# Kernel optimization log

Measured on AMD Instinct MI355X. Metric: run time of the kernel, lower is better.

The kernel has to match this reference:

```python
import jax, jax.numpy as jnp
import numpy as np

B, C_IN, C_OUT, H, W = 8, 64, 64, 128, 128
KH = KW = 3
K = KH * KW
PAD = 1


def setup_inputs() -> dict:
    key = jax.random.key(0)
    k1, k2, k3, k4 = jax.random.split(key, 4)
    inputs = {
        "input": jax.random.normal(k1, (B, C_IN, H, W), dtype=jnp.float32),
        "offset_and_mask": jax.random.normal(k2, (B, 3 * K, H, W), dtype=jnp.float32),
        "weight": jax.random.normal(k3, (C_OUT, C_IN, KH, KW), dtype=jnp.float32) * (1.0 / np.sqrt(C_IN * K)),
        "bias": jax.random.normal(k4, (C_OUT,), dtype=jnp.float32) * 0.1,
    }
    return inputs


def _dcnv2(x, offset_and_mask, weight, bias):
    b, c, h, w = x.shape
    co = weight.shape[0]
    # offset layout: first 2K channels are (dy, dx) pairs per kernel point, last K are mask logits
    off = offset_and_mask[:, : 2 * K].reshape(b, K, 2, h, w)
    mask = jax.nn.sigmoid(offset_and_mask[:, 2 * K :])  # [b, K, h, w]

    # base sampling grid for 3x3 conv, stride 1, pad 1, dilation 1
    hh = jnp.arange(h, dtype=jnp.float32)
    ww = jnp.arange(w, dtype=jnp.float32)
    ky = (jnp.arange(K) // KW).astype(jnp.float32) - PAD  # [K]
    kx = (jnp.arange(K) % KW).astype(jnp.float32) - PAD
    base_y = hh[None, :, None] + ky[:, None, None]  # [K, h, 1]
    base_x = ww[None, None, :] + kx[:, None, None]  # [K, 1, w]
    ys = base_y + off[:, :, 0]  # [b, K, h, w]
    xs = base_x + off[:, :, 1]

    def sample_one(img, ys1, xs1):
        # img [c,h,w]; ys1, xs1 [K,h,w]; bilinear with zero padding outside
        y0 = jnp.floor(ys1).astype(jnp.int32)
        x0 = jnp.floor(xs1).astype(jnp.int32)
        y1, x1 = y0 + 1, x0 + 1
        wy = ys1 - y0.astype(jnp.float32)
        wx = xs1 - x0.astype(jnp.float32)
        img_flat = img.reshape(c, h * w)

        def gather(yi, xi):
            valid = ((yi >= 0) & (yi < h) & (xi >= 0) & (xi < w)).astype(img.dtype)
            flat = jnp.clip(yi, 0, h - 1) * w + jnp.clip(xi, 0, w - 1)  # [K,h,w]
            v = img_flat[:, flat.reshape(-1)].reshape(c, K, h, w)
            return v * valid[None]

        v00 = gather(y0, x0)
        v01 = gather(y0, x1)
        v10 = gather(y1, x0)
        v11 = gather(y1, x1)
        return (
            v00 * ((1 - wy) * (1 - wx))[None]
            + v01 * ((1 - wy) * wx)[None]
            + v10 * (wy * (1 - wx))[None]
            + v11 * (wy * wx)[None]
        )  # [c, K, h, w]

    sampled = jax.vmap(sample_one)(x, ys, xs)  # [b, c, K, h, w]
    sampled = sampled * mask[:, None]
    w_flat = weight.reshape(co, c, K)
    out = jnp.einsum("bckhw,ock->bohw", sampled, w_flat)
    return out + bias[None, :, None, None]


def reference(input, offset_and_mask, weight, bias):
    return _dcnv2(input, offset_and_mask, weight, bias)
```

## Files before the change

kernel.cpp:

```cpp
#include <hip/hip_runtime.h>

#define Bn 8
#define Cc 64
#define CO 64
#define Hh 128
#define Ww 128
#define Kk 9
#define HW (Hh*Ww)

typedef __attribute__((ext_vector_type(8))) short bf16x8;
typedef __attribute__((ext_vector_type(4))) float f32x4;

__device__ __forceinline__ short f2bf(float f) {
    unsigned u = __float_as_uint(f);
    u = (u + 0x7FFFu + ((u >> 16) & 1u)) >> 16;
    return (short)u;
}
__device__ __forceinline__ float bf2f(short s) {
    return __uint_as_float(((unsigned)(unsigned short)s) << 16);
}

__global__ __launch_bounds__(256) void transpose_in_kernel(
    const float* __restrict__ in, short* __restrict__ in_t)
{
    __shared__ float tile[64 * 65];
    int bid  = blockIdx.x;
    int xblk = bid & 1;
    int row  = bid >> 1;
    int y    = row & (Hh - 1);
    int b    = row >> 7;
    int x0   = xblk << 6;
    int t    = threadIdx.x;

    int x  = t & 63;
    int cq = t >> 6;
    const float* src = in + (size_t)b * Cc * HW + (size_t)y * Ww + x0;
#pragma unroll
    for (int i = 0; i < 16; ++i) {
        int c = cq * 16 + i;
        tile[c * 65 + x] = src[(size_t)c * HW + x];
    }
    __syncthreads();
    int c2 = t & 63;
    int xq = t >> 6;
    short* dst = in_t + ((size_t)(b * Hh + y) * Ww + x0) * Cc;
#pragma unroll
    for (int i = 0; i < 16; ++i) {
        int xx = xq * 16 + i;
        dst[(size_t)xx * Cc + c2] = f2bf(tile[c2 * 65 + xx]);
    }
}

__global__ __launch_bounds__(256) void prep_w_kernel(
    const float* __restrict__ w, short* __restrict__ w_t)
{
    int idx = blockIdx.x * 256 + threadIdx.x;
    if (idx < Kk * CO * Cc) {
        int k  = idx >> 12;
        int co = (idx >> 6) & 63;
        int c  = idx & 63;
        w_t[idx] = f2bf(w[((size_t)co * Cc + c) * Kk + k]);
    }
}

__global__ __launch_bounds__(256, 4) void dcn_main_kernel(
    const short* __restrict__ in_t,
    const float* __restrict__ offm,
    const short* __restrict__ w_t,
    const float* __restrict__ bias,
    float* __restrict__ out)
{
    __shared__ short s_S[2][64][72];
    __shared__ short s_W[2][64][72];

    int bid  = blockIdx.x;
    int xblk = bid & 1;
    int row  = bid >> 1;
    int y    = row & (Hh - 1);
    int b    = row >> 7;
    int x0   = xblk << 6;
    int t    = threadIdx.x;
    int l    = t & 63;
    int wv   = t >> 6;
    int p_sub = l >> 2;
    int chunk = l & 3;
    int px   = (wv << 4) + p_sub;

    const float* offb = offm + (size_t)b * 27 * HW + (size_t)y * Ww + x0 + px;
    const short* inb  = in_t + (size_t)b * HW * Cc;

    int wco = t >> 2;
    int wc0 = (t & 3) << 4;

    float offv[Kk][3];
#pragma unroll
    for (int k = 0; k < Kk; ++k) {
        offv[k][0] = offb[(size_t)(2 * k) * HW];
        offv[k][1] = offb[(size_t)(2 * k + 1) * HW];
        offv[k][2] = offb[(size_t)(18 + k) * HW];
    }

    f32x4 acc[4] = {{0.f,0.f,0.f,0.f},{0.f,0.f,0.f,0.f},{0.f,0.f,0.f,0.f},{0.f,0.f,0.f,0.f}};
    int lm = l & 15;
    int g  = l >> 4;

    bf16x8 r[4][2];
    float  cw[4];
    bf16x8 wr[2];

    auto stage_load = [&](int k) {
        float dy = offv[k][0], dx = offv[k][1], ml = offv[k][2];
        float m  = __builtin_amdgcn_rcpf(1.0f + __expf(-ml));

        float ys = (float)(y + (k / 3) - 1) + dy;
        float xs = (float)(x0 + px + (k % 3) - 1) + dx;
        float yf = floorf(ys), xf = floorf(xs);
        int y0i = (int)yf, x0i = (int)xf;
        float wy = ys - yf, wx = xs - xf;

        bool vy0 = (unsigned)y0i < (unsigned)Hh;
        bool vy1 = (unsigned)(y0i + 1) < (unsigned)Hh;
        bool vx0 = (unsigned)x0i < (unsigned)Ww;
        bool vx1 = (unsigned)(x0i + 1) < (unsigned)Ww;

        int cy0 = min(max(y0i, 0), Hh - 1);
        int cy1 = min(max(y0i + 1, 0), Hh - 1);
        int cx0 = min(max(x0i, 0), Ww - 1);
        int cx1 = min(max(x0i + 1, 0), Ww - 1);

        cw[0] = (vy0 && vx0) ? (1.0f - wy) * (1.0f - wx) * m : 0.0f;
        cw[1] = (vy0 && vx1) ? (1.0f - wy) * wx * m : 0.0f;
        cw[2] = (vy1 && vx0) ? wy * (1.0f - wx) * m : 0.0f;
        cw[3] = (vy1 && vx1) ? wy * wx * m : 0.0f;

        int i00 = cy0 * Ww + cx0, i01 = cy0 * Ww + cx1;
        int i10 = cy1 * Ww + cx0, i11 = cy1 * Ww + cx1;
        int idx0[4] = {i00, i01, i10, i11};

#pragma unroll
        for (int cc = 0; cc < 4; ++cc) {
            const short* p = inb + (size_t)idx0[cc] * Cc + (chunk << 3);
            r[cc][0] = *(const bf16x8*)p;
            r[cc][1] = *(const bf16x8*)(p + 32);
        }
        const short* wk = w_t + (size_t)k * (CO * Cc) + 16 * t;
        wr[0] = *(const bf16x8*)(wk);
        wr[1] = *(const bf16x8*)(wk + 8);
    };

    auto stage_finish = [&](int nb) {
        float a0[8], a1[8];
#pragma unroll
        for (int j = 0; j < 8; ++j) { a0[j] = 0.0f; a1[j] = 0.0f; }
#pragma unroll
        for (int cc = 0; cc < 4; ++cc) {
            float w = cw[cc];
#pragma unroll
            for (int j = 0; j < 8; ++j) {
                a0[j] += w * bf2f(r[cc][0][j]);
                a1[j] += w * bf2f(r[cc][1][j]);
            }
        }
        union { bf16x8 v; short s[8]; } o0, o1;
#pragma unroll
        for (int j = 0; j < 8; ++j) { o0.s[j] = f2bf(a0[j]); o1.s[j] = f2bf(a1[j]); }
        *(bf16x8*)&s_S[nb][px][(chunk << 3)]      = o0.v;
        *(bf16x8*)&s_S[nb][px][32 + (chunk << 3)] = o1.v;

        *(bf16x8*)&s_W[nb][wco][wc0]     = wr[0];
        *(bf16x8*)&s_W[nb][wco][wc0 + 8] = wr[1];
    };

    stage_load(0);
    stage_finish(0);
    __syncthreads();

#pragma unroll
    for (int k = 0; k < Kk; ++k) {
        int cb = k & 1;
        if (k < Kk - 1) stage_load(k + 1);

        bf16x8 b0 = *(const bf16x8*)&s_S[cb][(wv << 4) + lm][(g << 3)];
        bf16x8 b1 = *(const bf16x8*)&s_S[cb][(wv << 4) + lm][32 + (g << 3)];
#pragma unroll
        for (int f = 0; f < 4; ++f) {
            bf16x8 A0 = *(const bf16x8*)&s_W[cb][(f << 4) + lm][(g << 3)];
            bf16x8 A1 = *(const bf16x8*)&s_W[cb][(f << 4) + lm][32 + (g << 3)];
            acc[f] = __builtin_amdgcn_mfma_f32_16x16x32_bf16(A0, b0, acc[f], 0, 0, 0);
            acc[f] = __builtin_amdgcn_mfma_f32_16x16x32_bf16(A1, b1, acc[f], 0, 0, 0);
        }
        if (k < Kk - 1) stage_finish(cb ^ 1);
        __syncthreads();
    }

    float* outb = out + (size_t)b * CO * HW + (size_t)y * Ww + x0 + (wv << 4) + lm;
#pragma unroll
    for (int f = 0; f < 4; ++f) {
#pragma unroll
        for (int rr = 0; rr < 4; ++rr) {
            int co = (f << 4) + (g << 2) + rr;
            outb[(size_t)co * HW] = acc[f][rr] + bias[co];
        }
    }
}

extern "C" void kernel_launch(void* const* d_in, const int* in_sizes, int n_in,
                              void* d_out, int out_size, void* d_ws, size_t ws_size,
                              hipStream_t stream)
{
    const float* in   = (const float*)d_in[0];
    const float* offm = (const float*)d_in[1];
    const float* w    = (const float*)d_in[2];
    const float* bias = (const float*)d_in[3];
    float* out = (float*)d_out;

    short* in_t = (short*)d_ws;
    short* w_t  = in_t + (size_t)Bn * HW * Cc;

    transpose_in_kernel<<<Bn * Hh * 2, 256, 0, stream>>>(in, in_t);
    prep_w_kernel<<<(Kk * CO * Cc + 255) / 256, 256, 0, stream>>>(w, w_t);
    dcn_main_kernel<<<Bn * Hh * 2, 256, 0, stream>>>(in_t, offm, w_t, bias, out);
}
```

Measured before the change: 59.85 us.

## Build MFMA B operands directly in registers, dropping the sampled-tile LDS round trip

```diff
diff --git a/kernel.cpp b/kernel.cpp
--- a/kernel.cpp
+++ b/kernel.cpp
@@ -16,8 +16,11 @@
     u = (u + 0x7FFFu + ((u >> 16) & 1u)) >> 16;
     return (short)u;
 }
-__device__ __forceinline__ float bf2f(short s) {
-    return __uint_as_float(((unsigned)(unsigned short)s) << 16);
+
+__device__ __forceinline__ unsigned cvt_pk_bf16(float lo, float hi) {
+    unsigned d;
+    asm("v_cvt_pk_bf16_f32 %0, %1, %2" : "=v"(d) : "v"(lo), "v"(hi));
+    return d;
 }
 
 __global__ __launch_bounds__(256) void transpose_in_kernel(
@@ -70,7 +73,6 @@
     const float* __restrict__ bias,
     float* __restrict__ out)
 {
-    __shared__ short s_S[2][64][72];
     __shared__ short s_W[2][64][72];
 
     int bid  = blockIdx.x;
@@ -82,9 +84,9 @@
     int t    = threadIdx.x;
     int l    = t & 63;
     int wv   = t >> 6;
-    int p_sub = l >> 2;
-    int chunk = l & 3;
-    int px   = (wv << 4) + p_sub;
+    int lm   = l & 15;
+    int g    = l >> 4;
+    int px   = (wv << 4) + lm;
 
     const float* offb = offm + (size_t)b * 27 * HW + (size_t)y * Ww + x0 + px;
     const short* inb  = in_t + (size_t)b * HW * Cc;
@@ -101,14 +103,16 @@
     }
 
     f32x4 acc[4] = {{0.f,0.f,0.f,0.f},{0.f,0.f,0.f,0.f},{0.f,0.f,0.f,0.f},{0.f,0.f,0.f,0.f}};
-    int lm = l & 15;
-    int g  = l >> 4;
-
-    bf16x8 r[4][2];
-    float  cw[4];
-    bf16x8 wr[2];
+
+    uint4 r[4][2];
+    uint4 wq[2];
+    float cw[4];
 
     auto stage_load = [&](int k) {
+        const uint4* wk = (const uint4*)(w_t + (size_t)k * (CO * Cc) + 16 * t);
+        wq[0] = wk[0];
+        wq[1] = wk[1];
+
         float dy = offv[k][0], dx = offv[k][1], ml = offv[k][2];
         float m  = __builtin_amdgcn_rcpf(1.0f + __expf(-ml));
 
@@ -133,55 +137,60 @@
         cw[2] = (vy1 && vx0) ? wy * (1.0f - wx) * m : 0.0f;
         cw[3] = (vy1 && vx1) ? wy * wx * m : 0.0f;
 
-        int i00 = cy0 * Ww + cx0, i01 = cy0 * Ww + cx1;
-        int i10 = cy1 * Ww + cx0, i11 = cy1 * Ww + cx1;
-        int idx0[4] = {i00, i01, i10, i11};
-
+        int idx[4] = {cy0 * Ww + cx0, cy0 * Ww + cx1, cy1 * Ww + cx0, cy1 * Ww + cx1};
 #pragma unroll
         for (int cc = 0; cc < 4; ++cc) {
-            const short* p = inb + (size_t)idx0[cc] * Cc + (chunk << 3);
-            r[cc][0] = *(const bf16x8*)p;
-            r[cc][1] = *(const bf16x8*)(p + 32);
-        }
-        const short* wk = w_t + (size_t)k * (CO * Cc) + 16 * t;
-        wr[0] = *(const bf16x8*)(wk);
-        wr[1] = *(const bf16x8*)(wk + 8);
+            const short* p = inb + (size_t)idx[cc] * Cc + (g << 3);
+            r[cc][0] = *(const uint4*)p;
+            r[cc][1] = *(const uint4*)(p + 32);
+        }
     };
 
-    auto stage_finish = [&](int nb) {
+    auto w_store = [&](int nb) {
+        *(uint4*)&s_W[nb][wco][wc0]     = wq[0];
+        *(uint4*)&s_W[nb][wco][wc0 + 8] = wq[1];
+    };
+
+    bf16x8 b0, b1;
+    auto blend_pack = [&]() {
         float a0[8], a1[8];
 #pragma unroll
         for (int j = 0; j < 8; ++j) { a0[j] = 0.0f; a1[j] = 0.0f; }
 #pragma unroll
         for (int cc = 0; cc < 4; ++cc) {
             float w = cw[cc];
-#pragma unroll
-            for (int j = 0; j < 8; ++j) {
-                a0[j] += w * bf2f(r[cc][0][j]);
-                a1[j] += w * bf2f(r[cc][1][j]);
+            unsigned q0[4] = {r[cc][0].x, r[cc][0].y, r[cc][0].z, r[cc][0].w};
+            unsigned q1[4] = {r[cc][1].x, r[cc][1].y, r[cc][1].z, r[cc][1].w};
+#pragma unroll
+            for (int d = 0; d < 4; ++d) {
+                a0[2*d]   = fmaf(w, __uint_as_float(q0[d] << 16),         a0[2*d]);
+                a0[2*d+1] = fmaf(w, __uint_as_float(q0[d] & 0xffff0000u), a0[2*d+1]);
+                a1[2*d]   = fmaf(w, __uint_as_float(q1[d] << 16),         a1[2*d]);
+                a1[2*d+1] = fmaf(w, __uint_as_float(q1[d] & 0xffff0000u), a1[2*d+1]);
             }
         }
-        union { bf16x8 v; short s[8]; } o0, o1;
-#pragma unroll
-        for (int j = 0; j < 8; ++j) { o0.s[j] = f2bf(a0[j]); o1.s[j] = f2bf(a1[j]); }
-        *(bf16x8*)&s_S[nb][px][(chunk << 3)]      = o0.v;
-        *(bf16x8*)&s_S[nb][px][32 + (chunk << 3)] = o1.v;
-
-        *(bf16x8*)&s_W[nb][wco][wc0]     = wr[0];
-        *(bf16x8*)&s_W[nb][wco][wc0 + 8] = wr[1];
+        union { unsigned d[4]; bf16x8 v; } p0, p1;
+#pragma unroll
+        for (int j = 0; j < 4; ++j) {
+            p0.d[j] = cvt_pk_bf16(a0[2*j], a0[2*j+1]);
+            p1.d[j] = cvt_pk_bf16(a1[2*j], a1[2*j+1]);
+        }
+        b0 = p0.v;
+        b1 = p1.v;
     };
 
     stage_load(0);
-    stage_finish(0);
+    w_store(0);
     __syncthreads();
 
 #pragma unroll
     for (int k = 0; k < Kk; ++k) {
         int cb = k & 1;
-        if (k < Kk - 1) stage_load(k + 1);
-
-        bf16x8 b0 = *(const bf16x8*)&s_S[cb][(wv << 4) + lm][(g << 3)];
-        bf16x8 b1 = *(const bf16x8*)&s_S[cb][(wv << 4) + lm][32 + (g << 3)];
+        blend_pack();
+        if (k < Kk - 1) {
+            stage_load(k + 1);
+            w_store(cb ^ 1);
+        }
 #pragma unroll
         for (int f = 0; f < 4; ++f) {
             bf16x8 A0 = *(const bf16x8*)&s_W[cb][(f << 4) + lm][(g << 3)];
@@ -189,8 +198,7 @@
             acc[f] = __builtin_amdgcn_mfma_f32_16x16x32_bf16(A0, b0, acc[f], 0, 0, 0);
             acc[f] = __builtin_amdgcn_mfma_f32_16x16x32_bf16(A1, b1, acc[f], 0, 0, 0);
         }
-        if (k < Kk - 1) stage_finish(cb ^ 1);
-        __syncthreads();
+        if (k < Kk - 1) __syncthreads();
     }
 
     float* outb = out + (size_t)b * CO * HW + (size_t)y * Ww + x0 + (wv << 4) + lm;
```

Result: slower. 96.44 us (+61.1%).
